# Optimization experiments

Hardware: AMD Instinct MI355X
Metric: run time of the kernel (lower is better)

Reference implementation:

```python
import jax, jax.numpy as jnp
import numpy as np

N, E, R, K1, F = 50000, 400000, 1000, 1000, 128
DEPTH, HEADS = 1, 2

def _l2norm(x, axis):
    n = jnp.sqrt(jnp.maximum(jnp.sum(x * x, axis=axis, keepdims=True), 1e-12))
    return x / n

def _segment_softmax(logits, seg, num_segments):
    m = jax.ops.segment_max(logits, seg, num_segments=num_segments)
    e = jnp.exp(logits - m[seg])
    s = jax.ops.segment_sum(e, seg, num_segments=num_segments)
    return e / s[seg]

def setup_inputs() -> dict:
    rng = np.random.RandomState(0)
    # adjacency: nodes 0..K1-1 have exactly one edge (long-tail), rest random rows
    rows = np.concatenate([np.arange(K1), rng.randint(K1, N, size=E - K1)])
    cols = rng.randint(0, N, size=E)
    order = np.lexsort((cols, rows))
    adj = np.stack([rows, cols], axis=1)[order].astype(np.int32)  # [E,2] sorted by row
    self_nodes_idx = np.arange(K1, dtype=np.int32)
    neights_node_idxs = adj[:K1, 1].astype(np.int32)  # neighbor of each degree-1 node
    sparse_indices = np.stack([np.arange(E), rng.randint(0, R, size=E)], axis=1).astype(np.int32)
    sparse_val = (rng.rand(E).astype(np.float32) * 0.5 + 0.5)
    key = jax.random.key(0)
    k = jax.random.split(key, 5)
    return {
        'features': jax.random.normal(k[0], (N, F), jnp.float32),
        'rel_emb': jax.random.normal(k[1], (R, F), jnp.float32),
        'sparse_val': jnp.asarray(sparse_val),
        'attn_kernels': jax.random.normal(k[2], (DEPTH, HEADS, F), jnp.float32) * (1.0 / np.sqrt(F)),
        'proxy': jax.random.normal(k[3], (64, F * (DEPTH + 1)), jnp.float32) * 0.1,
        'gate_kernel': jax.random.normal(k[4], (F * (DEPTH + 1), F * (DEPTH + 1)), jnp.float32) * (1.0 / np.sqrt(F * (DEPTH + 1))),
        'adj_indices': jnp.asarray(adj),
        'sparse_indices': jnp.asarray(sparse_indices),
        'self_nodes_idx': jnp.asarray(self_nodes_idx),
        'neights_node_idxs': jnp.asarray(neights_node_idxs),
    }

def reference(features, rel_emb, sparse_val, attn_kernels, proxy, gate_kernel,
              adj_indices, sparse_indices, self_nodes_idx, neights_node_idxs):
    row = adj_indices[:, 0]
    col = adj_indices[:, 1]
    feats = features  # activation is linear (None)
    outputs = [feats]
    for l in range(DEPTH):
        # per-triple relation embedding: sparse (E,R) @ rel_emb -> (E,F)
        rels_sum = jax.ops.segment_sum(sparse_val[:, None] * rel_emb[sparse_indices[:, 1]],
                                       sparse_indices[:, 0], num_segments=E)
        rels_norm = _l2norm(rels_sum, axis=1)  # l2 normalize rows
        neighs = feats[col]  # [E,F] gather
        # Householder reflection of neighbor features by relation direction
        neighs = neighs - 2.0 * jnp.sum(neighs * rels_norm, axis=1, keepdims=True) * rels_norm
        head_feats = []
        for head in range(HEADS):
            att_logits = rels_sum @ attn_kernels[l, head]  # [E]
            att = _segment_softmax(att_logits, row, N)  # sparse softmax per destination node
            nf = jax.ops.segment_sum(neighs * att[:, None], row, num_segments=N)  # [N,F]
            if head == 1:
                # long-tail fix: degree-1 nodes copy their single neighbor's aggregated feature
                nf = nf.at[self_nodes_idx].set(nf[neights_node_idxs])
            head_feats.append(nf)
        feats = jnp.mean(jnp.stack(head_feats, axis=0), axis=0)
        outputs.append(feats)
    out = jnp.concatenate(outputs, axis=-1)  # [N, F*(DEPTH+1)]
    proxy_att = jax.nn.softmax(_l2norm(out, axis=-1) @ _l2norm(proxy, axis=-1).T, axis=-1)  # [N,64]
    proxy_feature = out - proxy_att @ proxy
    gate = jax.nn.sigmoid(proxy_feature @ gate_kernel)
    return gate * out + (1.0 - gate) * proxy_feature
```

## Files before the change

kernel.cpp:

```cpp
#include <hip/hip_runtime.h>
#include <math.h>

constexpr int N  = 50000;
constexpr int E  = 400000;
constexpr int R  = 1000;
constexpr int K1 = 1000;
constexpr int F  = 128;
constexpr int OUTC = 256;
constexpr int P  = 64;

typedef _Float16 f16x8 __attribute__((ext_vector_type(8)));
typedef _Float16 f16x4 __attribute__((ext_vector_type(4)));
typedef _Float16 f16x2 __attribute__((ext_vector_type(2)));
typedef float f32x4 __attribute__((ext_vector_type(4)));

#if __has_builtin(__builtin_amdgcn_fdot2)
#define FDOT2(a, b, c) __builtin_amdgcn_fdot2((a), (b), (c), false)
#else
#define FDOT2(a, b, c) fmaf((float)(a)[0], (float)(b)[0], fmaf((float)(a)[1], (float)(b)[1], (c)))
#endif

__device__ inline float waveReduceSum(float v) {
#pragma unroll
    for (int m = 32; m >= 1; m >>= 1) v += __shfl_xor(v, m, 64);
    return v;
}

constexpr int B_FEATSH = 3125;
constexpr int B_REL    = 250;
constexpr int B_SEG    = 1563;
constexpr int B_PSC    = 16;
constexpr int B_PGF    = 64;

__global__ __launch_bounds__(256) void prep_a(
        const float* __restrict__ feats, const float* __restrict__ rel_emb,
        const float* __restrict__ attn,  const float* __restrict__ proxy,
        const float* __restrict__ G,     const int* __restrict__ adj,
        _Float16* __restrict__ featsH,   _Float16* __restrict__ relnormH,
        float* __restrict__ dotr, int* __restrict__ nstart, int* __restrict__ nend,
        float* __restrict__ pscale, float* __restrict__ PGf) {
    int b = blockIdx.x, tid = threadIdx.x;
    if (b < B_FEATSH) {
        int idx = b * 256 + tid;
        float4 x0 = ((const float4*)feats)[2 * idx];
        float4 x1 = ((const float4*)feats)[2 * idx + 1];
        f16x8 h;
        h[0] = (_Float16)x0.x; h[1] = (_Float16)x0.y;
        h[2] = (_Float16)x0.z; h[3] = (_Float16)x0.w;
        h[4] = (_Float16)x1.x; h[5] = (_Float16)x1.y;
        h[6] = (_Float16)x1.z; h[7] = (_Float16)x1.w;
        ((f16x8*)featsH)[idx] = h;
    } else if (b < B_FEATSH + B_REL) {
        int r = (b - B_FEATSH) * 4 + (tid >> 6);
        int lane = tid & 63;
        float2 v  = ((const float2*)(rel_emb + (size_t)r * F))[lane];
        float2 a0 = ((const float2*)attn)[lane];
        float2 a1 = ((const float2*)attn)[64 + lane];
        float ss = waveReduceSum(v.x * v.x + v.y * v.y);
        float d0 = waveReduceSum(v.x * a0.x + v.y * a0.y);
        float d1 = waveReduceSum(v.x * a1.x + v.y * a1.y);
        float sc = rsqrtf(fmaxf(ss, 1e-12f));
        f16x2 h; h[0] = (_Float16)(v.x * sc); h[1] = (_Float16)(v.y * sc);
        ((f16x2*)(relnormH + (size_t)r * F))[lane] = h;
        if (lane == 0) { dotr[2 * r] = d0; dotr[2 * r + 1] = d1; }
    } else if (b < B_FEATSH + B_REL + B_SEG) {
        int e = (b - B_FEATSH - B_REL) * 256 + tid;
        if (e < E) {
            int lane = tid & 63;
            int row = ((const int2*)adj)[e].x;
            int prev = __shfl_up(row, 1, 64);
            if (lane == 0) prev = (e > 0) ? ((const int2*)adj)[e - 1].x : -1;
            int nxt = __shfl_down(row, 1, 64);
            if (lane == 63 && e + 1 < E) nxt = ((const int2*)adj)[e + 1].x;
            if (prev != row) {
                nstart[row] = e;
                for (int rr = prev + 1; rr < row; ++rr) { nstart[rr] = e; nend[rr] = e; }
            }
            if (e == E - 1) {
                nend[row] = E;
                for (int rr = row + 1; rr < N; ++rr) { nstart[rr] = E; nend[rr] = E; }
            } else if (nxt != row) {
                nend[row] = e + 1;
            }
        }
    } else if (b < B_FEATSH + B_REL + B_SEG + B_PSC) {
        int j = (b - B_FEATSH - B_REL - B_SEG) * 4 + (tid >> 6);
        int lane = tid & 63;
        float4 p = ((const float4*)(proxy + (size_t)j * OUTC))[lane];
        float ss = waveReduceSum(p.x * p.x + p.y * p.y + p.z * p.z + p.w * p.w);
        if (lane == 0) pscale[j] = rsqrtf(fmaxf(ss, 1e-12f));
    } else {
        int p = b - (B_FEATSH + B_REL + B_SEG + B_PSC);
        int c = tid;
        float s = 0.f;
        for (int k = 0; k < OUTC; ++k)
            s = fmaf(proxy[(size_t)p * OUTC + k], G[(size_t)k * OUTC + c], s);
        PGf[(size_t)p * OUTC + c] = s;
    }
}

constexpr int NB_NODE = N / 4;
constexpr int NB_FRAG = 56;

__global__ __launch_bounds__(256) void node_frag(
        const _Float16* __restrict__ featsH,
        const _Float16* __restrict__ relnormH,
        const float* __restrict__ dotr,
        const int* __restrict__ adj,
        const int* __restrict__ sidx,
        const float* __restrict__ val,
        const int* __restrict__ nstart,
        const int* __restrict__ nend,
        const float* __restrict__ G,
        const float* __restrict__ proxy,
        const float* __restrict__ pscale,
        const float* __restrict__ PGf,
        _Float16* __restrict__ nf0,
        _Float16* __restrict__ nf1,
        f16x8* __restrict__ Gh, f16x8* __restrict__ pnH,
        f16x8* __restrict__ pxH, f16x8* __restrict__ pgH) {
    if (blockIdx.x >= NB_NODE) {
        int u = (blockIdx.x - NB_NODE) * 4 + (threadIdx.x >> 6);
        int L = threadIdx.x & 63;
        int q = L >> 4, m = L & 15;
        f16x8 h;
        if (u < 128) {
            int kk = u >> 4, cg = u & 15;
            int n = cg * 16 + m;
#pragma unroll
            for (int j = 0; j < 8; ++j)
                h[j] = (_Float16)G[(size_t)(kk * 32 + q * 8 + j) * OUTC + n];
            Gh[(size_t)u * 64 + L] = h;
        } else if (u < 160) {
            int idx = u - 128;
            int kk = idx >> 2, w = idx & 3;
            int n = w * 16 + m;
            float sc = pscale[n];
#pragma unroll
            for (int j = 0; j < 8; ++j)
                h[j] = (_Float16)(proxy[(size_t)n * OUTC + kk * 32 + q * 8 + j] * sc);
            pnH[(size_t)idx * 64 + L] = h;
        } else if (u < 192) {
            int idx = u - 160;
            int kk = idx >> 4, cg = idx & 15;
            int n = cg * 16 + m;
#pragma unroll
            for (int j = 0; j < 8; ++j)
                h[j] = (_Float16)proxy[(size_t)(kk * 32 + q * 8 + j) * OUTC + n];
            pxH[(size_t)idx * 64 + L] = h;
        } else {
            int idx = u - 192;
            int kk = idx >> 4, cg = idx & 15;
            int n = cg * 16 + m;
#pragma unroll
            for (int j = 0; j < 8; ++j)
                h[j] = (_Float16)(-PGf[(size_t)(kk * 32 + q * 8 + j) * OUTC + n]);
            pgH[(size_t)idx * 64 + L] = h;
        }
        return;
    }
    int n = blockIdx.x * 4 + (threadIdx.x >> 6);
    int lane = threadIdx.x & 63;
    int g = lane >> 4, gl = lane & 15;
    int start = nstart[n], end = nend[n];
    const int2* adj2 = (const int2*)adj;
    const int2* sx2  = (const int2*)sidx;
    float A0[8], A1[8];
#pragma unroll
    for (int j = 0; j < 8; ++j) { A0[j] = 0.f; A1[j] = 0.f; }
    float s0 = 0.f, s1 = 0.f;
    for (int e = start + g; e < end; e += 8) {
        int eB = e + 4;
        bool hasB = (eB < end);
        int eBc = hasB ? eB : e;
        int colA = adj2[e].y,   colB = adj2[eBc].y;
        int relA = sx2[e].y,    relB = sx2[eBc].y;
        float vA = val[e],      vB = val[eBc];
        float2 drA = ((const float2*)dotr)[relA];
        float2 drB = ((const float2*)dotr)[relB];
        float wA0 = __expf(vA * drA.x), wA1 = __expf(vA * drA.y);
        float wB0 = hasB ? __expf(vB * drB.x) : 0.f;
        float wB1 = hasB ? __expf(vB * drB.y) : 0.f;
        s0 += wA0 + wB0; s1 += wA1 + wB1;
        f16x8 fAv = ((const f16x8*)(featsH   + (size_t)colA * F))[gl];
        f16x8 rAv = ((const f16x8*)(relnormH + (size_t)relA * F))[gl];
        f16x8 fBv = ((const f16x8*)(featsH   + (size_t)colB * F))[gl];
        f16x8 rBv = ((const f16x8*)(relnormH + (size_t)relB * F))[gl];
        const f16x2* fA2 = (const f16x2*)&fAv;
        const f16x2* rA2 = (const f16x2*)&rAv;
        const f16x2* fB2 = (const f16x2*)&fBv;
        const f16x2* rB2 = (const f16x2*)&rBv;
        float pdA = 0.f, pdB = 0.f;
#pragma unroll
        for (int j = 0; j < 4; ++j) {
            pdA = FDOT2(fA2[j], rA2[j], pdA);
            pdB = FDOT2(fB2[j], rB2[j], pdB);
        }
        pdA += __shfl_xor(pdA, 1, 64); pdB += __shfl_xor(pdB, 1, 64);
        pdA += __shfl_xor(pdA, 2, 64); pdB += __shfl_xor(pdB, 2, 64);
        pdA += __shfl_xor(pdA, 4, 64); pdB += __shfl_xor(pdB, 4, 64);
        pdA += __shfl_xor(pdA, 8, 64); pdB += __shfl_xor(pdB, 8, 64);
        _Float16 tAh = (_Float16)(2.f * pdA), tBh = (_Float16)(2.f * pdB);
        f16x2 tA2; tA2[0] = tAh; tA2[1] = tAh;
        f16x2 tB2; tB2[0] = tBh; tB2[1] = tBh;
#pragma unroll
        for (int j = 0; j < 4; ++j) {
            f16x2 rxA = fA2[j] - tA2 * rA2[j];
            f16x2 rxB = fB2[j] - tB2 * rB2[j];
            float x0 = (float)rxA[0], x1 = (float)rxA[1];
            float y0 = (float)rxB[0], y1 = (float)rxB[1];
            A0[2*j]   = fmaf(wA0, x0, A0[2*j]);   A0[2*j]   = fmaf(wB0, y0, A0[2*j]);
            A0[2*j+1] = fmaf(wA0, x1, A0[2*j+1]); A0[2*j+1] = fmaf(wB0, y1, A0[2*j+1]);
            A1[2*j]   = fmaf(wA1, x0, A1[2*j]);   A1[2*j]   = fmaf(wB1, y0, A1[2*j]);
            A1[2*j+1] = fmaf(wA1, x1, A1[2*j+1]); A1[2*j+1] = fmaf(wB1, y1, A1[2*j+1]);
        }
    }
#pragma unroll
    for (int j = 0; j < 8; ++j) {
        A0[j] += __shfl_xor(A0[j], 16, 64); A0[j] += __shfl_xor(A0[j], 32, 64);
        A1[j] += __shfl_xor(A1[j], 16, 64); A1[j] += __shfl_xor(A1[j], 32, 64);
    }
    s0 += __shfl_xor(s0, 16, 64); s0 += __shfl_xor(s0, 32, 64);
    s1 += __shfl_xor(s1, 16, 64); s1 += __shfl_xor(s1, 32, 64);
    float i0 = (s0 > 0.f) ? 1.f / s0 : 0.f;
    float i1 = (s1 > 0.f) ? 1.f / s1 : 0.f;
    if (g == 0) {
        f16x8 h0, h1;
#pragma unroll
        for (int j = 0; j < 8; ++j) {
            h0[j] = (_Float16)(A0[j] * i0);
            h1[j] = (_Float16)(A1[j] * i1);
        }
        ((f16x8*)(nf0 + (size_t)n * F))[gl] = h0;
        ((f16x8*)(nf1 + (size_t)n * F))[gl] = h1;
    }
}

constexpr int RT = 2;
__global__ __launch_bounds__(256, 4) void proxy_gate(
        const _Float16* __restrict__ featsH,
        const _Float16* __restrict__ nf0,
        const _Float16* __restrict__ nf1,
        const int* __restrict__ neigh,
        const f16x8* __restrict__ pnH,
        const f16x8* __restrict__ pxH,
        const f16x8* __restrict__ Gh,
        const f16x8* __restrict__ pgH,
        float* __restrict__ out) {
    constexpr int LDA = 68;
    __shared__ __align__(16) f16x8 outH[RT * 8 * 64];
    __shared__ __align__(16) float attL[RT * 16 * LDA];
    __shared__ float scaleL[RT * 16];
    int tid = threadIdx.x;
    int w = tid >> 6, lane = tid & 63;
    int quad = lane >> 4, m = lane & 15;
    size_t row0 = (size_t)blockIdx.x * (RT * 16);

    {
        int bm = tid >> 4, gl = tid & 15;
#pragma unroll
        for (int t = 0; t < RT; ++t) {
            int n = (int)row0 + t * 16 + bm;
            float ss;
            f16x8 h1, h2;
            if (n < N) {
                ss = 0.f;
                h1 = ((const f16x8*)(featsH + (size_t)n * F))[gl];
#pragma unroll
                for (int j = 0; j < 8; ++j) { float x = (float)h1[j]; ss += x * x; }
                int sel = (n < K1) ? neigh[n] : n;
                f16x8 a  = ((const f16x8*)(nf0 + (size_t)n   * F))[gl];
                f16x8 b2 = ((const f16x8*)(nf1 + (size_t)sel * F))[gl];
#pragma unroll
                for (int j = 0; j < 8; ++j) {
                    float v = 0.5f * ((float)a[j] + (float)b2[j]);
                    h2[j] = (_Float16)v;
                    ss += v * v;
                }
            } else {
#pragma unroll
                for (int j = 0; j < 8; ++j) { h1[j] = (_Float16)0.f; h2[j] = (_Float16)0.f; }
                ss = 1.f;
            }
            outH[(t * 8 +     (gl >> 2)) * 64 + (gl & 3) * 16 + bm] = h1;
            outH[(t * 8 + 4 + (gl >> 2)) * 64 + (gl & 3) * 16 + bm] = h2;
            ss += __shfl_xor(ss, 1, 64); ss += __shfl_xor(ss, 2, 64);
            ss += __shfl_xor(ss, 4, 64); ss += __shfl_xor(ss, 8, 64);
            if (gl == 0) scaleL[t * 16 + bm] = rsqrtf(fmaxf(ss, 1e-12f));
        }
    }
    __syncthreads();

    f32x4 lacc[RT];
    f32x4 zacc[RT][4];
#pragma unroll
    for (int t = 0; t < RT; ++t) {
        lacc[t] = (f32x4){0,0,0,0};
#pragma unroll
        for (int c = 0; c < 4; ++c) zacc[t][c] = (f32x4){0,0,0,0};
    }
#pragma unroll
    for (int kk = 0; kk < 8; ++kk) {
        f16x8 pb  = pnH[(size_t)(kk * 4 + w) * 64 + lane];
        f16x8 gb0 = Gh[(size_t)(kk * 16 + w +  0) * 64 + lane];
        f16x8 gb1 = Gh[(size_t)(kk * 16 + w +  4) * 64 + lane];
        f16x8 gb2 = Gh[(size_t)(kk * 16 + w +  8) * 64 + lane];
        f16x8 gb3 = Gh[(size_t)(kk * 16 + w + 12) * 64 + lane];
#pragma unroll
        for (int t = 0; t < RT; ++t) {
            f16x8 a = outH[(t * 8 + kk) * 64 + lane];
            lacc[t]    = __builtin_amdgcn_mfma_f32_16x16x32_f16(a, pb,  lacc[t],    0, 0, 0);
            zacc[t][0] = __builtin_amdgcn_mfma_f32_16x16x32_f16(a, gb0, zacc[t][0], 0, 0, 0);
            zacc[t][1] = __builtin_amdgcn_mfma_f32_16x16x32_f16(a, gb1, zacc[t][1], 0, 0, 0);
            zacc[t][2] = __builtin_amdgcn_mfma_f32_16x16x32_f16(a, gb2, zacc[t][2], 0, 0, 0);
            zacc[t][3] = __builtin_amdgcn_mfma_f32_16x16x32_f16(a, gb3, zacc[t][3], 0, 0, 0);
        }
    }
#pragma unroll
    for (int t = 0; t < RT; ++t)
#pragma unroll
        for (int i = 0; i < 4; ++i) {
            int r = t * 16 + quad * 4 + i;
            attL[r * LDA + w * 16 + m] = lacc[t][i] * scaleL[r];
        }
    __syncthreads();

#pragma unroll
    for (int t = 0; t < RT; ++t)
#pragma unroll
        for (int i = 0; i < 4; ++i) {
            int r = t * 16 + 4 * w + i;
            float e = __expf(attL[r * LDA + lane]);
            float s = waveReduceSum(e);
            attL[r * LDA + lane] = e / s;
        }
    __syncthreads();

    f32x4 qacc[RT][4];
#pragma unroll
    for (int t = 0; t < RT; ++t)
#pragma unroll
        for (int c = 0; c < 4; ++c) qacc[t][c] = (f32x4){0,0,0,0};
#pragma unroll
    for (int kk = 0; kk < 2; ++kk) {
        f16x8 a[RT];
#pragma unroll
        for (int t = 0; t < RT; ++t) {
            const float4* ap = (const float4*)&attL[(t * 16 + m) * LDA + kk * 32 + quad * 8];
            float4 x = ap[0], y = ap[1];
            a[t][0]=(_Float16)x.x; a[t][1]=(_Float16)x.y; a[t][2]=(_Float16)x.z; a[t][3]=(_Float16)x.w;
            a[t][4]=(_Float16)y.x; a[t][5]=(_Float16)y.y; a[t][6]=(_Float16)y.z; a[t][7]=(_Float16)y.w;
        }
#pragma unroll
        for (int cgi = 0; cgi < 4; ++cgi) {
            int cg = w + 4 * cgi;
            f16x8 bx = pxH[(size_t)(kk * 16 + cg) * 64 + lane];
            f16x8 bg = pgH[(size_t)(kk * 16 + cg) * 64 + lane];
#pragma unroll
            for (int t = 0; t < RT; ++t) {
                qacc[t][cgi] = __builtin_amdgcn_mfma_f32_16x16x32_f16(a[t], bx, qacc[t][cgi], 0, 0, 0);
                zacc[t][cgi] = __builtin_amdgcn_mfma_f32_16x16x32_f16(a[t], bg, zacc[t][cgi], 0, 0, 0);
            }
        }
    }

    const _Float16* outHs = (const _Float16*)outH;
#pragma unroll
    for (int t = 0; t < RT; ++t) {
        if ((int)row0 + t * 16 >= N) break;
#pragma unroll
        for (int cgi = 0; cgi < 4; ++cgi) {
            int cg = w + 4 * cgi;
            int c = cg * 16 + m;
            int kkc = cg >> 1;
            int qc = ((cg & 1) << 1) | (m >> 3);
            int j = m & 7;
#pragma unroll
            for (int i = 0; i < 4; ++i) {
                int r15 = quad * 4 + i;
                float ov = (float)outHs[(((t * 8 + kkc) * 64 + qc * 16 + r15) << 3) + j];
                float gate = 1.f / (1.f + __expf(-zacc[t][cgi][i]));
                size_t n = row0 + t * 16 + r15;
                out[n * OUTC + c] = ov - (1.f - gate) * qacc[t][cgi][i];
            }
        }
    }
}

extern "C" void kernel_launch(void* const* d_in, const int* in_sizes, int n_in,
                              void* d_out, int out_size, void* d_ws, size_t ws_size,
                              hipStream_t stream) {
    const float* features   = (const float*)d_in[0];
    const float* rel_emb    = (const float*)d_in[1];
    const float* sparse_val = (const float*)d_in[2];
    const float* attn       = (const float*)d_in[3];
    const float* proxy      = (const float*)d_in[4];
    const float* gateK      = (const float*)d_in[5];
    const int*   adj        = (const int*)d_in[6];
    const int*   sidx       = (const int*)d_in[7];
    const int*   neigh      = (const int*)d_in[9];
    float* out = (float*)d_out;

    char* ws = (char*)d_ws;
    size_t off = 0;
    auto alloc = [&](size_t bytes) -> void* {
        void* p = ws + off;
        off += (bytes + 255) & ~(size_t)255;
        return p;
    };
    _Float16* relnormH = (_Float16*)alloc((size_t)R * F * 2);
    float*    dotr     = (float*)alloc((size_t)R * 2 * 4);
    float*    pscale   = (float*)alloc((size_t)P * 4);
    float*    PGf      = (float*)alloc((size_t)P * OUTC * 4);
    f16x8*    Gh       = (f16x8*)alloc((size_t)128 * 64 * 16);
    f16x8*    pnH      = (f16x8*)alloc((size_t)32 * 64 * 16);
    f16x8*    pxH      = (f16x8*)alloc((size_t)32 * 64 * 16);
    f16x8*    pgH      = (f16x8*)alloc((size_t)32 * 64 * 16);
    _Float16* featsH   = (_Float16*)alloc((size_t)N * F * 2);
    int*      nstart   = (int*)alloc((size_t)N * 4);
    int*      nend     = (int*)alloc((size_t)N * 4);
    _Float16* nf0      = (_Float16*)alloc((size_t)N * F * 2);
    _Float16* nf1      = (_Float16*)alloc((size_t)N * F * 2);

    prep_a<<<B_FEATSH + B_REL + B_SEG + B_PSC + B_PGF, 256, 0, stream>>>(
        features, rel_emb, attn, proxy, gateK, adj,
        featsH, relnormH, dotr, nstart, nend, pscale, PGf);
    node_frag<<<NB_NODE + NB_FRAG, 256, 0, stream>>>(
        featsH, relnormH, dotr, adj, sidx, sparse_val, nstart, nend,
        gateK, proxy, pscale, PGf,
        nf0, nf1, Gh, pnH, pxH, pgH);
    proxy_gate<<<(N + RT * 16 - 1) / (RT * 16), 256, 0, stream>>>(
        featsH, nf0, nf1, neigh, pnH, pxH, Gh, pgH, out);
}
```

Baseline: 178.2 us.

## Double row tile in proxy_gate and split gate GEMM into two column halves

Raises rows per block from 32 to 64, so each weight fragment loaded from global memory feeds twice as many MFMAs. The gate-kernel GEMM is no longer computed alongside the proxy-logit GEMM; it moves after the softmax and runs in two output-column halves, each combined with the proxy correction and written out. This keeps accumulator register pressure bounded at the larger tile, at the cost of reloading the outH A-fragments twice and lowering occupancy (launch bounds go from 4 to 2 blocks per CU).

```diff
diff --git a/kernel.cpp b/kernel.cpp
--- a/kernel.cpp
+++ b/kernel.cpp
@@ -236,8 +236,8 @@
     }
 }
 
-constexpr int RT = 2;
-__global__ __launch_bounds__(256, 4) void proxy_gate(
+constexpr int RT = 4;
+__global__ __launch_bounds__(256, 2) void proxy_gate(
         const _Float16* __restrict__ featsH,
         const _Float16* __restrict__ nf0,
         const _Float16* __restrict__ nf1,
@@ -291,38 +291,27 @@
     }
     __syncthreads();
 
-    f32x4 lacc[RT];
-    f32x4 zacc[RT][4];
-#pragma unroll
-    for (int t = 0; t < RT; ++t) {
-        lacc[t] = (f32x4){0,0,0,0};
-#pragma unroll
-        for (int c = 0; c < 4; ++c) zacc[t][c] = (f32x4){0,0,0,0};
-    }
-#pragma unroll
-    for (int kk = 0; kk < 8; ++kk) {
-        f16x8 pb  = pnH[(size_t)(kk * 4 + w) * 64 + lane];
-        f16x8 gb0 = Gh[(size_t)(kk * 16 + w +  0) * 64 + lane];
-        f16x8 gb1 = Gh[(size_t)(kk * 16 + w +  4) * 64 + lane];
-        f16x8 gb2 = Gh[(size_t)(kk * 16 + w +  8) * 64 + lane];
-        f16x8 gb3 = Gh[(size_t)(kk * 16 + w + 12) * 64 + lane];
-#pragma unroll
-        for (int t = 0; t < RT; ++t) {
-            f16x8 a = outH[(t * 8 + kk) * 64 + lane];
-            lacc[t]    = __builtin_amdgcn_mfma_f32_16x16x32_f16(a, pb,  lacc[t],    0, 0, 0);
-            zacc[t][0] = __builtin_amdgcn_mfma_f32_16x16x32_f16(a, gb0, zacc[t][0], 0, 0, 0);
-            zacc[t][1] = __builtin_amdgcn_mfma_f32_16x16x32_f16(a, gb1, zacc[t][1], 0, 0, 0);
-            zacc[t][2] = __builtin_amdgcn_mfma_f32_16x16x32_f16(a, gb2, zacc[t][2], 0, 0, 0);
-            zacc[t][3] = __builtin_amdgcn_mfma_f32_16x16x32_f16(a, gb3, zacc[t][3], 0, 0, 0);
-        }
-    }
-#pragma unroll
-    for (int t = 0; t < RT; ++t)
-#pragma unroll
-        for (int i = 0; i < 4; ++i) {
-            int r = t * 16 + quad * 4 + i;
-            attL[r * LDA + w * 16 + m] = lacc[t][i] * scaleL[r];
-        }
+    {
+        f32x4 lacc[RT];
+#pragma unroll
+        for (int t = 0; t < RT; ++t) lacc[t] = (f32x4){0,0,0,0};
+#pragma unroll
+        for (int kk = 0; kk < 8; ++kk) {
+            f16x8 pb = pnH[(size_t)(kk * 4 + w) * 64 + lane];
+#pragma unroll
+            for (int t = 0; t < RT; ++t) {
+                f16x8 a = outH[(t * 8 + kk) * 64 + lane];
+                lacc[t] = __builtin_amdgcn_mfma_f32_16x16x32_f16(a, pb, lacc[t], 0, 0, 0);
+            }
+        }
+#pragma unroll
+        for (int t = 0; t < RT; ++t)
+#pragma unroll
+            for (int i = 0; i < 4; ++i) {
+                int r = t * 16 + quad * 4 + i;
+                attL[r * LDA + w * 16 + m] = lacc[t][i] * scaleL[r];
+            }
+    }
     __syncthreads();
 
 #pragma unroll
@@ -336,52 +325,68 @@
         }
     __syncthreads();
 
-    f32x4 qacc[RT][4];
-#pragma unroll
-    for (int t = 0; t < RT; ++t)
-#pragma unroll
-        for (int c = 0; c < 4; ++c) qacc[t][c] = (f32x4){0,0,0,0};
-#pragma unroll
-    for (int kk = 0; kk < 2; ++kk) {
-        f16x8 a[RT];
+    const _Float16* outHs = (const _Float16*)outH;
+#pragma unroll
+    for (int hf = 0; hf < 2; ++hf) {
+        f32x4 zacc[RT][2], qacc[RT][2];
+#pragma unroll
+        for (int t = 0; t < RT; ++t)
+#pragma unroll
+            for (int c = 0; c < 2; ++c) {
+                zacc[t][c] = (f32x4){0,0,0,0};
+                qacc[t][c] = (f32x4){0,0,0,0};
+            }
+#pragma unroll
+        for (int kk = 0; kk < 8; ++kk) {
+            f16x8 gb0 = Gh[(size_t)(kk * 16 + w + 8 * hf + 0) * 64 + lane];
+            f16x8 gb1 = Gh[(size_t)(kk * 16 + w + 8 * hf + 4) * 64 + lane];
+#pragma unroll
+            for (int t = 0; t < RT; ++t) {
+                f16x8 a = outH[(t * 8 + kk) * 64 + lane];
+                zacc[t][0] = __builtin_amdgcn_mfma_f32_16x16x32_f16(a, gb0, zacc[t][0], 0, 0, 0);
+                zacc[t][1] = __builtin_amdgcn_mfma_f32_16x16x32_f16(a, gb1, zacc[t][1], 0, 0, 0);
+            }
+        }
+#pragma unroll
+        for (int kk = 0; kk < 2; ++kk) {
+            f16x8 a[RT];
+#pragma unroll
+            for (int t = 0; t < RT; ++t) {
+                const float4* ap = (const float4*)&attL[(t * 16 + m) * LDA + kk * 32 + quad * 8];
+                float4 x = ap[0], y = ap[1];
+                a[t][0]=(_Float16)x.x; a[t][1]=(_Float16)x.y; a[t][2]=(_Float16)x.z; a[t][3]=(_Float16)x.w;
+                a[t][4]=(_Float16)y.x; a[t][5]=(_Float16)y.y; a[t][6]=(_Float16)y.z; a[t][7]=(_Float16)y.w;
+            }
+#pragma unroll
+            for (int cgi = 0; cgi < 2; ++cgi) {
+                int cg = w + 4 * cgi + 8 * hf;
+                f16x8 bx = pxH[(size_t)(kk * 16 + cg) * 64 + lane];
+                f16x8 bg = pgH[(size_t)(kk * 16 + cg) * 64 + lane];
+#pragma unroll
+                for (int t = 0; t < RT; ++t) {
+                    qacc[t][cgi] = __builtin_amdgcn_mfma_f32_16x16x32_f16(a[t], bx, qacc[t][cgi], 0, 0, 0);
+                    zacc[t][cgi] = __builtin_amdgcn_mfma_f32_16x16x32_f16(a[t], bg, zacc[t][cgi], 0, 0, 0);
+                }
+            }
+        }
 #pragma unroll
         for (int t = 0; t < RT; ++t) {
-            const float4* ap = (const float4*)&attL[(t * 16 + m) * LDA + kk * 32 + quad * 8];
-            float4 x = ap[0], y = ap[1];
-            a[t][0]=(_Float16)x.x; a[t][1]=(_Float16)x.y; a[t][2]=(_Float16)x.z; a[t][3]=(_Float16)x.w;
-            a[t][4]=(_Float16)y.x; a[t][5]=(_Float16)y.y; a[t][6]=(_Float16)y.z; a[t][7]=(_Float16)y.w;
-        }
-#pragma unroll
-        for (int cgi = 0; cgi < 4; ++cgi) {
-            int cg = w + 4 * cgi;
-            f16x8 bx = pxH[(size_t)(kk * 16 + cg) * 64 + lane];
-            f16x8 bg = pgH[(size_t)(kk * 16 + cg) * 64 + lane];
-#pragma unroll
-            for (int t = 0; t < RT; ++t) {
-                qacc[t][cgi] = __builtin_amdgcn_mfma_f32_16x16x32_f16(a[t], bx, qacc[t][cgi], 0, 0, 0);
-                zacc[t][cgi] = __builtin_amdgcn_mfma_f32_16x16x32_f16(a[t], bg, zacc[t][cgi], 0, 0, 0);
-            }
-        }
-    }
-
-    const _Float16* outHs = (const _Float16*)outH;
-#pragma unroll
-    for (int t = 0; t < RT; ++t) {
-        if ((int)row0 + t * 16 >= N) break;
-#pragma unroll
-        for (int cgi = 0; cgi < 4; ++cgi) {
-            int cg = w + 4 * cgi;
-            int c = cg * 16 + m;
-            int kkc = cg >> 1;
-            int qc = ((cg & 1) << 1) | (m >> 3);
-            int j = m & 7;
-#pragma unroll
-            for (int i = 0; i < 4; ++i) {
-                int r15 = quad * 4 + i;
-                float ov = (float)outHs[(((t * 8 + kkc) * 64 + qc * 16 + r15) << 3) + j];
-                float gate = 1.f / (1.f + __expf(-zacc[t][cgi][i]));
-                size_t n = row0 + t * 16 + r15;
-                out[n * OUTC + c] = ov - (1.f - gate) * qacc[t][cgi][i];
+            if ((int)row0 + t * 16 >= N) break;
+#pragma unroll
+            for (int cgi = 0; cgi < 2; ++cgi) {
+                int cg = w + 4 * cgi + 8 * hf;
+                int c = cg * 16 + m;
+                int kkc = cg >> 1;
+                int qc = ((cg & 1) << 1) | (m >> 3);
+                int j = m & 7;
+#pragma unroll
+                for (int i = 0; i < 4; ++i) {
+                    int r15 = quad * 4 + i;
+                    float ov = (float)outHs[(((t * 8 + kkc) * 64 + qc * 16 + r15) << 3) + j];
+                    float gate = 1.f / (1.f + __expf(-zacc[t][cgi][i]));
+                    size_t n = row0 + t * 16 + r15;
+                    out[n * OUTC + c] = ov - (1.f - gate) * qacc[t][cgi][i];
+                }
             }
         }
     }
```

After: 180.3 us. About the same (+1.1%).
